# Optimization experiments

Hardware: AMD Instinct MI355X
Metric: run time of the kernel (lower is better)

Reference implementation:

```python
import jax, jax.numpy as jnp
import numpy as np

# ---- static config (mirrors HashEncoderHyFluid.__init__) ----
MIN_RES = np.array([16, 16, 16, 16], dtype=np.float64)
MAX_RES = np.array([256, 256, 256, 128], dtype=np.float64)
NUM_SCALES = 16
MAX_PARAMS = 2 ** 19
F = 2  # features_per_level
N_QUERIES = 1_000_000
PRIMES = np.array([1, 2654435761, 805459861, 3674653429], dtype=np.uint32)
# 16 corner offsets of the 4D hypercube, bit d of idx selects low/high along dim d
BITS = np.array([[(i >> d) & 1 for d in range(4)] for i in range(16)], dtype=np.int32)  # (16,4)


def build_config():
    b = np.exp((np.log(MAX_RES) - np.log(MIN_RES)) / (NUM_SCALES - 1))
    shapes, sizes, indicators, offsets = [], [], [], []
    total = 0
    for s in range(NUM_SCALES):
        res = np.ceil(MIN_RES * np.power(b, s)).astype(np.int64)
        raw = int(res[0] + 1) * int(res[1] + 1) * int(res[2] + 1) * int(res[3] + 1)
        p = raw if raw % 8 == 0 else ((raw + 7) // 8) * 8
        p = min(MAX_PARAMS, p)
        shapes.append(res)
        sizes.append(p)
        indicators.append(1 if raw <= p else 0)
        offsets.append(total)
        total += p * F
    return shapes, sizes, indicators, offsets, total


SHAPES, SIZES, INDICATORS, OFFSETS, TOTAL_HASH_SIZE = build_config()  # total = 15205344


def setup_inputs() -> dict:
    key = jax.random.key(0)
    k1, k2 = jax.random.split(key)
    xyzt = jax.random.uniform(k1, (N_QUERIES, 4), dtype=jnp.float32)  # coords in [0,1)
    hash_table = (jax.random.uniform(k2, (TOTAL_HASH_SIZE,), dtype=jnp.float32) * 2.0 - 1.0) * 0.001
    return {"xyzt": xyzt, "hash_table": hash_table}


def _encode_scale(xyzt, hash_table, res, size, indicator, offset):
    # xyzt: (N,4) in [0,1]; res: np int64 (4,)
    resf = jnp.asarray(res.astype(np.float32))
    pos = xyzt * resf                      # (N,4) grid-space position
    grid = jnp.floor(pos)
    frac = pos - grid                      # (N,4)
    grid = grid.astype(jnp.int32)
    corners = grid[:, None, :] + jnp.asarray(BITS)[None, :, :]          # (N,16,4)
    hi = jnp.asarray(BITS, jnp.float32)[None, :, :]                     # (1,16,4)
    w = jnp.prod(hi * frac[:, None, :] + (1.0 - hi) * (1.0 - frac[:, None, :]), axis=-1)  # (N,16)
    cu = corners.astype(jnp.uint32)
    if indicator == 1:
        # dense linear indexing: strides = cumprod(res+1), wrapping at uint32 like taichi
        strides = np.cumprod(np.concatenate([[1], (res + 1)[:3]])).astype(np.uint32)
        idx = jnp.sum(cu * jnp.asarray(strides), axis=-1)               # (N,16) uint32, wraps
    else:
        # xor hash with large primes
        h = cu[..., 0] * jnp.uint32(PRIMES[0])
        for d in range(1, 4):
            h = h ^ (cu[..., d] * jnp.uint32(PRIMES[d]))
        idx = h
    idx = (idx % jnp.uint32(size)).astype(jnp.int32)
    base = offset + idx * F                                             # (N,16)
    feats = hash_table[base[..., None] + jnp.arange(F)]                 # (N,16,F)
    return jnp.einsum("nc,ncf->nf", w, feats)                           # (N,F)


def reference(xyzt, hash_table):
    outs = []
    for s in range(NUM_SCALES):
        outs.append(_encode_scale(xyzt, hash_table, SHAPES[s], SIZES[s], INDICATORS[s], OFFSETS[s]))
    return jnp.concatenate(outs, axis=-1)  # (N, NUM_SCALES * F)
```

## Files before the change

kernel.cpp:

```cpp
#include <hip/hip_runtime.h>
#include <cstdint>
#include <cmath>


#define NSCALES 16
#define TPB 256
#define BINS 65536
#define QPB 128

struct Cfg {
  float    res[NSCALES][4];
  uint32_t key[NSCALES][4];
  uint32_t mask[NSCALES];
  int      offset[NSCALES];
  int      dense[NSCALES];
};

typedef float v4f __attribute__((ext_vector_type(4)));
typedef float v2f __attribute__((ext_vector_type(2)));

__device__ __forceinline__ uint32_t bucket_key(float x, float y, float z, float w)
{
  uint32_t bx = (uint32_t)(x * 16.f); bx = bx > 15u ? 15u : bx;
  uint32_t by = (uint32_t)(y * 16.f); by = by > 15u ? 15u : by;
  uint32_t bz = (uint32_t)(z * 16.f); bz = bz > 15u ? 15u : bz;
  uint32_t bt = (uint32_t)(w * 16.f); bt = bt > 15u ? 15u : bt;
  uint32_t k = 0;
#pragma unroll
  for (int b = 0; b < 4; ++b) {
    k |= ((bx >> b) & 1u) << (4 * b + 0);
    k |= ((by >> b) & 1u) << (4 * b + 1);
    k |= ((bz >> b) & 1u) << (4 * b + 2);
    k |= ((bt >> b) & 1u) << (4 * b + 3);
  }
  return k;
}

__global__ __launch_bounds__(TPB) void hist_kernel(
    const float* __restrict__ xyzt, uint32_t* __restrict__ hist, int N)
{
  const int i = blockIdx.x * TPB + threadIdx.x;
  if (i >= N) return;
  const v4f c = *(reinterpret_cast<const v4f*>(xyzt) + i);
  atomicAdd(&hist[bucket_key(c.x, c.y, c.z, c.w)], 1u);
}

__global__ __launch_bounds__(1024) void scan_kernel(
    const uint32_t* __restrict__ hist, uint32_t* __restrict__ boff)
{
  __shared__ uint32_t part[1024];
  const int t = threadIdx.x;
  const int base = t * (BINS / 1024);
  uint32_t s = 0;
  for (int j = 0; j < BINS / 1024; ++j) s += hist[base + j];
  part[t] = s;
  __syncthreads();
  for (int off = 1; off < 1024; off <<= 1) {
    uint32_t v = (t >= off) ? part[t - off] : 0u;
    __syncthreads();
    part[t] += v;
    __syncthreads();
  }
  uint32_t run = part[t] - s;
  for (int j = 0; j < BINS / 1024; ++j) {
    boff[base + j] = run;
    run += hist[base + j];
  }
}

__global__ __launch_bounds__(TPB) void scatter_kernel(
    const float* __restrict__ xyzt,
    const uint32_t* __restrict__ boff, uint32_t* __restrict__ cur,
    uint32_t* __restrict__ perm, float* __restrict__ c_sorted, int N)
{
  const int i = blockIdx.x * TPB + threadIdx.x;
  if (i >= N) return;
  const v4f c = *(reinterpret_cast<const v4f*>(xyzt) + i);
  const uint32_t k = bucket_key(c.x, c.y, c.z, c.w);
  const uint32_t pos = boff[k] + atomicAdd(&cur[k], 1u);
  perm[pos] = (uint32_t)i;
  *(reinterpret_cast<v4f*>(c_sorted) + pos) = c;
}

__global__ __launch_bounds__(TPB) void gather_kernel(
    const float*  __restrict__ coords,
    const float*  __restrict__ table,
    float2*       __restrict__ ws,
    int N, int s_base, Cfg cfg)
{
  const int s = (int)blockIdx.y + s_base;
  const int q = blockIdx.x * TPB + threadIdx.x;
  if (q >= N) return;
  const v4f c = *(reinterpret_cast<const v4f*>(coords) + q);

  const float rx = cfg.res[s][0], ry = cfg.res[s][1];
  const float rz = cfg.res[s][2], rw = cfg.res[s][3];
  const uint32_t K0 = cfg.key[s][0], K1 = cfg.key[s][1];
  const uint32_t K2 = cfg.key[s][2], K3 = cfg.key[s][3];

  const float px = c.x * rx, py = c.y * ry, pz = c.z * rz, pw = c.w * rw;
  const float gx = floorf(px), gy = floorf(py), gz = floorf(pz), gw = floorf(pw);
  const float fx = px - gx, fy = py - gy, fz = pz - gz, fw = pw - gw;
  const uint32_t ix = (uint32_t)(int)gx, iy = (uint32_t)(int)gy;
  const uint32_t iz = (uint32_t)(int)gz, iw = (uint32_t)(int)gw;

  const uint32_t x0 = ix * K0, x1 = x0 + K0;
  const uint32_t y0 = iy * K1, y1 = y0 + K1;
  const uint32_t z0 = iz * K2, z1 = z0 + K2;
  const uint32_t u0 = iw * K3, u1 = u0 + K3;

  const float wx0 = 1.f - fx, wy0 = 1.f - fy, wz0 = 1.f - fz, ww0 = 1.f - fw;
  const float wA[4] = { wx0 * wy0, fx * wy0, wx0 * fy, fx * fy };
  const float wB[4] = { wz0 * ww0, fz * ww0, wz0 * fw, fz * fw };

  const float*  tbf = table + cfg.offset[s];
  const float2* __restrict__ tb  = reinterpret_cast<const float2*>(tbf);
  const float4* __restrict__ tb4 = reinterpret_cast<const float4*>(tbf);

  float a0 = 0.f, a1 = 0.f;
  if (cfg.dense[s]) {
    const uint32_t hA[4] = { x0 + y0, x1 + y0, x0 + y1, x1 + y1 };
    const uint32_t hB[4] = { z0 + u0, z1 + u0, z0 + u1, z1 + u1 };
    uint32_t idx[16];
#pragma unroll
    for (int i = 0; i < 16; ++i) idx[i] = hA[i & 3] + hB[i >> 2];
    float2 v[16];
#pragma unroll
    for (int i = 0; i < 16; ++i) v[i] = tb[idx[i]];
#pragma unroll
    for (int i = 0; i < 16; ++i) {
      const float w = wA[i & 3] * wB[i >> 2];
      a0 = fmaf(w, v[i].x, a0);
      a1 = fmaf(w, v[i].y, a1);
    }
  } else {
    const uint32_t msk = cfg.mask[s];
    if ((ix & 1u) == 0u) {
      const uint32_t yv[2] = { y0, y1 };
      const uint32_t zw[4] = { z0 ^ u0, z1 ^ u0, z0 ^ u1, z1 ^ u1 };
      uint32_t p[8];
#pragma unroll
      for (int j = 0; j < 8; ++j)
        p[j] = (x0 ^ yv[j & 1] ^ zw[j >> 1]) & msk;
      float4 v[8];
#pragma unroll
      for (int j = 0; j < 8; ++j) v[j] = tb4[p[j] >> 1];
#pragma unroll
      for (int j = 0; j < 8; ++j) {
        const int jy = j & 1, jz = j >> 1;
        const uint32_t sel = p[j] & 1u;
        const float wlo = wA[2 * jy]     * wB[jz];
        const float whi = wA[2 * jy + 1] * wB[jz];
        const float l0 = sel ? v[j].z : v[j].x, l1 = sel ? v[j].w : v[j].y;
        const float h0 = sel ? v[j].x : v[j].z, h1 = sel ? v[j].y : v[j].w;
        a0 = fmaf(wlo, l0, fmaf(whi, h0, a0));
        a1 = fmaf(wlo, l1, fmaf(whi, h1, a1));
      }
    } else {
      const uint32_t hA[4] = { x0 ^ y0, x1 ^ y0, x0 ^ y1, x1 ^ y1 };
      const uint32_t hB[4] = { z0 ^ u0, z1 ^ u0, z0 ^ u1, z1 ^ u1 };
      uint32_t idx[16];
#pragma unroll
      for (int i = 0; i < 16; ++i) idx[i] = (hA[i & 3] ^ hB[i >> 2]) & msk;
      float2 v[16];
#pragma unroll
      for (int i = 0; i < 16; ++i) v[i] = tb[idx[i]];
#pragma unroll
      for (int i = 0; i < 16; ++i) {
        const float w = wA[i & 3] * wB[i >> 2];
        a0 = fmaf(w, v[i].x, a0);
        a1 = fmaf(w, v[i].y, a1);
      }
    }
  }
  ws[(size_t)s * N + q] = make_float2(a0, a1);
}

__global__ __launch_bounds__(TPB) void transpose_perm(
    const float2*   __restrict__ ws,
    const uint32_t* __restrict__ perm,
    float*          __restrict__ out,
    int N)
{
  __shared__ float2 st[NSCALES][QPB + 1];
  const int t  = threadIdx.x;
  const int q0 = blockIdx.x * QPB;
#pragma unroll
  for (int i = 0; i < (NSCALES * QPB) / TPB; ++i) {
    const int idx = i * TPB + t;
    const int sc  = idx >> 7;
    const int qi  = idx & (QPB - 1);
    const int q   = q0 + qi;
    st[sc][qi] = ws[(size_t)sc * N + (q < N ? q : N - 1)];
  }
  __syncthreads();
#pragma unroll
  for (int i = 0; i < (QPB * 8) / TPB; ++i) {
    const int g  = i * TPB + t;
    const int qi = g >> 3;
    const int h  = g & 7;
    const int q  = q0 + qi;
    if (q < N) {
      const float2 a = st[2 * h][qi];
      const float2 b = st[2 * h + 1][qi];
      const uint32_t pq = perm[q];
      v4f val = { a.x, a.y, b.x, b.y };
      __builtin_nontemporal_store(val, (v4f*)(out + (size_t)pq * 32 + h * 4));
    }
  }
}

__global__ __launch_bounds__(TPB) void transpose_kernel(
    const float2* __restrict__ ws,
    float*        __restrict__ out,
    int N)
{
  __shared__ float2 st[NSCALES][TPB + 1];
  const int t  = threadIdx.x;
  const int q  = blockIdx.x * TPB + t;
  const int ql = q < N ? q : N - 1;
#pragma unroll
  for (int s = 0; s < NSCALES; ++s)
    st[s][t] = ws[(size_t)s * N + ql];
  __syncthreads();
  const int base = blockIdx.x * (TPB * 2 * NSCALES);
#pragma unroll
  for (int it = 0; it < 8; ++it) {
    const int G  = it * 1024 + t * 4;
    const int qi = G >> 5;
    const int s0 = (G & 31) >> 1;
    if (blockIdx.x * TPB + qi < N) {
      const float2 a = st[s0][qi];
      const float2 b = st[s0 + 1][qi];
      v4f val = { a.x, a.y, b.x, b.y };
      __builtin_nontemporal_store(val, (v4f*)(out + base + G));
    }
  }
}

__global__ __launch_bounds__(TPB) void hashenc_fused(
    const float4* __restrict__ xyzt,
    const float*  __restrict__ table,
    float*        __restrict__ out,
    int N, Cfg cfg)
{
  __shared__ float2 st[NSCALES][TPB + 1];
  const int t  = threadIdx.x;
  const int q  = blockIdx.x * TPB + t;
  const int ql = q < N ? q : N - 1;
  const float4 c = xyzt[ql];
#pragma unroll 1
  for (int s = 0; s < NSCALES; ++s) {
    const float rx = cfg.res[s][0], ry = cfg.res[s][1];
    const float rz = cfg.res[s][2], rw = cfg.res[s][3];
    const uint32_t K0 = cfg.key[s][0], K1 = cfg.key[s][1];
    const uint32_t K2 = cfg.key[s][2], K3 = cfg.key[s][3];
    const float px = c.x * rx, py = c.y * ry, pz = c.z * rz, pw = c.w * rw;
    const float gx = floorf(px), gy = floorf(py), gz = floorf(pz), gw = floorf(pw);
    const float fx = px - gx, fy = py - gy, fz = pz - gz, fw = pw - gw;
    const uint32_t ix = (uint32_t)(int)gx, iy = (uint32_t)(int)gy;
    const uint32_t iz = (uint32_t)(int)gz, iw = (uint32_t)(int)gw;
    const uint32_t x0 = ix * K0, x1 = x0 + K0;
    const uint32_t y0 = iy * K1, y1 = y0 + K1;
    const uint32_t z0 = iz * K2, z1 = z0 + K2;
    const uint32_t u0 = iw * K3, u1 = u0 + K3;
    const float wx0 = 1.f - fx, wy0 = 1.f - fy, wz0 = 1.f - fz, ww0 = 1.f - fw;
    const float wA[4] = { wx0 * wy0, fx * wy0, wx0 * fy, fx * fy };
    const float wB[4] = { wz0 * ww0, fz * ww0, wz0 * fw, fz * fw };
    const float2* __restrict__ tb =
        reinterpret_cast<const float2*>(table + cfg.offset[s]);
    float a0 = 0.f, a1 = 0.f;
    if (cfg.dense[s]) {
      const uint32_t hA[4] = { x0 + y0, x1 + y0, x0 + y1, x1 + y1 };
      const uint32_t hB[4] = { z0 + u0, z1 + u0, z0 + u1, z1 + u1 };
#pragma unroll
      for (int i = 0; i < 16; ++i) {
        const uint32_t idx = hA[i & 3] + hB[i >> 2];
        const float2 v = tb[idx];
        const float w = wA[i & 3] * wB[i >> 2];
        a0 = fmaf(w, v.x, a0); a1 = fmaf(w, v.y, a1);
      }
    } else {
      const uint32_t msk = cfg.mask[s];
      const uint32_t hA[4] = { x0 ^ y0, x1 ^ y0, x0 ^ y1, x1 ^ y1 };
      const uint32_t hB[4] = { z0 ^ u0, z1 ^ u0, z0 ^ u1, z1 ^ u1 };
#pragma unroll
      for (int i = 0; i < 16; ++i) {
        const uint32_t idx = (hA[i & 3] ^ hB[i >> 2]) & msk;
        const float2 v = tb[idx];
        const float w = wA[i & 3] * wB[i >> 2];
        a0 = fmaf(w, v.x, a0); a1 = fmaf(w, v.y, a1);
      }
    }
    st[s][t] = make_float2(a0, a1);
  }
  __syncthreads();
  const int base = blockIdx.x * (TPB * 2 * NSCALES);
#pragma unroll
  for (int it = 0; it < 8; ++it) {
    const int G  = it * 1024 + t * 4;
    const int qi = G >> 5;
    const int s0 = (G & 31) >> 1;
    if (blockIdx.x * TPB + qi < N) {
      const float2 a = st[s0][qi];
      const float2 b = st[s0 + 1][qi];
      v4f val = { a.x, a.y, b.x, b.y };
      __builtin_nontemporal_store(val, (v4f*)(out + base + G));
    }
  }
}

static void build_cfg(Cfg& cfg)
{
  const double minr[4] = { 16.0, 16.0, 16.0, 16.0 };
  const double maxr[4] = { 256.0, 256.0, 256.0, 128.0 };
  const uint32_t primes[4] = { 1u, 2654435761u, 805459861u, 3674653429u };

  double b[4];
  for (int d = 0; d < 4; ++d)
    b[d] = ::exp((::log(maxr[d]) - ::log(minr[d])) / (double)(NSCALES - 1));

  long long total = 0;
  for (int s = 0; s < NSCALES; ++s) {
    long long res[4];
    for (int d = 0; d < 4; ++d)
      res[d] = (long long)::ceil(minr[d] * ::pow(b[d], (double)s));

    const long long raw =
        (res[0] + 1) * (res[1] + 1) * (res[2] + 1) * (res[3] + 1);
    long long p = (raw % 8 == 0) ? raw : ((raw + 7) / 8) * 8;
    if (p > 524288) p = 524288;
    const int ind = (raw <= p) ? 1 : 0;

    for (int d = 0; d < 4; ++d) cfg.res[s][d] = (float)res[d];
    if (ind) {
      cfg.key[s][0] = 1u;
      cfg.key[s][1] = (uint32_t)(res[0] + 1);
      cfg.key[s][2] = (uint32_t)((res[0] + 1) * (res[1] + 1));
      cfg.key[s][3] = (uint32_t)((res[0] + 1) * (res[1] + 1) * (res[2] + 1));
    } else {
      for (int d = 0; d < 4; ++d) cfg.key[s][d] = primes[d];
    }
    cfg.mask[s]   = (uint32_t)(p - 1);
    cfg.offset[s] = (int)total;
    cfg.dense[s]  = ind;
    total += p * 2;
  }
}

static inline size_t align_up(size_t v, size_t a) { return (v + a - 1) & ~(a - 1); }

extern "C" void kernel_launch(void* const* d_in, const int* in_sizes, int n_in,
                              void* d_out, int out_size, void* d_ws, size_t ws_size,
                              hipStream_t stream)
{
  const float* xyzt  = (const float*)d_in[0];
  const float* table = (const float*)d_in[1];
  float*       out   = (float*)d_out;
  const int N = in_sizes[0] / 4;

  Cfg cfg;
  build_cfg(cfg);

  const int qblocks = (N + TPB - 1) / TPB;

  size_t off = 0;
  const size_t perm_off = off;             off = align_up(off + (size_t)N * 4, 256);
  const size_t hist_off = off;             off += (size_t)BINS * 4;
  const size_t cur_off  = off;             off = align_up(off + (size_t)BINS * 4, 256);
  const size_t boff_off = off;             off = align_up(off + (size_t)BINS * 4, 256);
  const size_t cs_off   = align_up(off, 16);  off = cs_off + (size_t)N * 16;
  const size_t ws_off   = align_up(off, 16);
  const size_t need_sorted = ws_off + (size_t)N * NSCALES * sizeof(float2);
  const size_t need_plain  = (size_t)N * NSCALES * sizeof(float2);

  char* wsb = (char*)d_ws;

  if (ws_size >= need_sorted) {
    uint32_t* perm = (uint32_t*)(wsb + perm_off);
    uint32_t* hist = (uint32_t*)(wsb + hist_off);
    uint32_t* cur  = (uint32_t*)(wsb + cur_off);
    uint32_t* boff = (uint32_t*)(wsb + boff_off);
    float*    csrt = (float*)(wsb + cs_off);
    float2*   ws   = (float2*)(wsb + ws_off);

    hipMemsetAsync(hist, 0, (size_t)BINS * 8, stream);
    hipLaunchKernelGGL(hist_kernel, dim3(qblocks), dim3(TPB), 0, stream,
                       xyzt, hist, N);
    hipLaunchKernelGGL(scan_kernel, dim3(1), dim3(1024), 0, stream, hist, boff);
    hipLaunchKernelGGL(scatter_kernel, dim3(qblocks), dim3(TPB), 0, stream,
                       xyzt, boff, cur, perm, csrt, N);
    hipLaunchKernelGGL(gather_kernel, dim3(qblocks, NSCALES), dim3(TPB), 0,
                       stream, csrt, table, ws, N, 0, cfg);
    const int tblocks = (N + QPB - 1) / QPB;
    hipLaunchKernelGGL(transpose_perm, dim3(tblocks), dim3(TPB), 0, stream,
                       ws, perm, out, N);
  } else if (ws_size >= need_plain) {
    float2* ws = (float2*)d_ws;
    hipLaunchKernelGGL(gather_kernel, dim3(qblocks, NSCALES), dim3(TPB), 0,
                       stream, xyzt, table, ws, N, 0, cfg);
    hipLaunchKernelGGL(transpose_kernel, dim3(qblocks), dim3(TPB), 0,
                       stream, ws, out, N);
  } else {
    hipLaunchKernelGGL(hashenc_fused, dim3(qblocks), dim3(TPB), 0,
                       stream, (const float4*)xyzt, table, out, N, cfg);
  }
}
```

Baseline: 811.2 us.

## Merge bucket offsets into cursor array, interleave gathers, use nontemporal workspace I/O

The scan now writes exclusive bucket offsets straight into the atomic cursor array, so the scatter no longer reads a separate offset array and the memset shrinks to one histogram. The gather loops now compute each index, load and accumulate in one unrolled body instead of separate phases, which may reduce register pressure. Workspace writes in the gather and reads in the transpose use nontemporal hints to avoid polluting cache that the hash table lookups rely on. The compiler may already hoist the loads, so the loop restructuring could change little.

Result: no change. 808.9 us, median of 2 (-0.3%).

```diff
diff --git a/kernel.cpp b/kernel.cpp
--- a/kernel.cpp
+++ b/kernel.cpp
@@ -46,7 +46,7 @@
 }
 
 __global__ __launch_bounds__(1024) void scan_kernel(
-    const uint32_t* __restrict__ hist, uint32_t* __restrict__ boff)
+    const uint32_t* __restrict__ hist, uint32_t* __restrict__ cur)
 {
   __shared__ uint32_t part[1024];
   const int t = threadIdx.x;
@@ -63,21 +63,21 @@
   }
   uint32_t run = part[t] - s;
   for (int j = 0; j < BINS / 1024; ++j) {
-    boff[base + j] = run;
+    cur[base + j] = run;
     run += hist[base + j];
   }
 }
 
 __global__ __launch_bounds__(TPB) void scatter_kernel(
     const float* __restrict__ xyzt,
-    const uint32_t* __restrict__ boff, uint32_t* __restrict__ cur,
+    uint32_t* __restrict__ cur,
     uint32_t* __restrict__ perm, float* __restrict__ c_sorted, int N)
 {
   const int i = blockIdx.x * TPB + threadIdx.x;
   if (i >= N) return;
   const v4f c = *(reinterpret_cast<const v4f*>(xyzt) + i);
   const uint32_t k = bucket_key(c.x, c.y, c.z, c.w);
-  const uint32_t pos = boff[k] + atomicAdd(&cur[k], 1u);
+  const uint32_t pos = atomicAdd(&cur[k], 1u);
   perm[pos] = (uint32_t)i;
   *(reinterpret_cast<v4f*>(c_sorted) + pos) = c;
 }
@@ -121,59 +121,48 @@
   if (cfg.dense[s]) {
     const uint32_t hA[4] = { x0 + y0, x1 + y0, x0 + y1, x1 + y1 };
     const uint32_t hB[4] = { z0 + u0, z1 + u0, z0 + u1, z1 + u1 };
-    uint32_t idx[16];
-#pragma unroll
-    for (int i = 0; i < 16; ++i) idx[i] = hA[i & 3] + hB[i >> 2];
-    float2 v[16];
-#pragma unroll
-    for (int i = 0; i < 16; ++i) v[i] = tb[idx[i]];
 #pragma unroll
     for (int i = 0; i < 16; ++i) {
+      const uint32_t idx = hA[i & 3] + hB[i >> 2];
+      const float2 v = tb[idx];
       const float w = wA[i & 3] * wB[i >> 2];
-      a0 = fmaf(w, v[i].x, a0);
-      a1 = fmaf(w, v[i].y, a1);
+      a0 = fmaf(w, v.x, a0);
+      a1 = fmaf(w, v.y, a1);
     }
   } else {
     const uint32_t msk = cfg.mask[s];
     if ((ix & 1u) == 0u) {
       const uint32_t yv[2] = { y0, y1 };
       const uint32_t zw[4] = { z0 ^ u0, z1 ^ u0, z0 ^ u1, z1 ^ u1 };
-      uint32_t p[8];
-#pragma unroll
-      for (int j = 0; j < 8; ++j)
-        p[j] = (x0 ^ yv[j & 1] ^ zw[j >> 1]) & msk;
-      float4 v[8];
-#pragma unroll
-      for (int j = 0; j < 8; ++j) v[j] = tb4[p[j] >> 1];
 #pragma unroll
       for (int j = 0; j < 8; ++j) {
         const int jy = j & 1, jz = j >> 1;
-        const uint32_t sel = p[j] & 1u;
+        const uint32_t p  = (x0 ^ yv[jy] ^ zw[jz]) & msk;
+        const uint32_t e  = p & ~1u;
+        const uint32_t sel = p & 1u;
+        const float4 v = tb4[e >> 1];
         const float wlo = wA[2 * jy]     * wB[jz];
         const float whi = wA[2 * jy + 1] * wB[jz];
-        const float l0 = sel ? v[j].z : v[j].x, l1 = sel ? v[j].w : v[j].y;
-        const float h0 = sel ? v[j].x : v[j].z, h1 = sel ? v[j].y : v[j].w;
+        const float l0 = sel ? v.z : v.x, l1 = sel ? v.w : v.y;
+        const float h0 = sel ? v.x : v.z, h1 = sel ? v.y : v.w;
         a0 = fmaf(wlo, l0, fmaf(whi, h0, a0));
         a1 = fmaf(wlo, l1, fmaf(whi, h1, a1));
       }
     } else {
       const uint32_t hA[4] = { x0 ^ y0, x1 ^ y0, x0 ^ y1, x1 ^ y1 };
       const uint32_t hB[4] = { z0 ^ u0, z1 ^ u0, z0 ^ u1, z1 ^ u1 };
-      uint32_t idx[16];
-#pragma unroll
-      for (int i = 0; i < 16; ++i) idx[i] = (hA[i & 3] ^ hB[i >> 2]) & msk;
-      float2 v[16];
-#pragma unroll
-      for (int i = 0; i < 16; ++i) v[i] = tb[idx[i]];
 #pragma unroll
       for (int i = 0; i < 16; ++i) {
+        const uint32_t idx = (hA[i & 3] ^ hB[i >> 2]) & msk;
+        const float2 v = tb[idx];
         const float w = wA[i & 3] * wB[i >> 2];
-        a0 = fmaf(w, v[i].x, a0);
-        a1 = fmaf(w, v[i].y, a1);
+        a0 = fmaf(w, v.x, a0);
+        a1 = fmaf(w, v.y, a1);
       }
     }
   }
-  ws[(size_t)s * N + q] = make_float2(a0, a1);
+  v2f val = { a0, a1 };
+  __builtin_nontemporal_store(val, (v2f*)&ws[(size_t)s * N + q]);
 }
 
 __global__ __launch_bounds__(TPB) void transpose_perm(
@@ -191,7 +180,9 @@
     const int sc  = idx >> 7;
     const int qi  = idx & (QPB - 1);
     const int q   = q0 + qi;
-    st[sc][qi] = ws[(size_t)sc * N + (q < N ? q : N - 1)];
+    const v2f tmp = __builtin_nontemporal_load(
+        reinterpret_cast<const v2f*>(&ws[(size_t)sc * N + (q < N ? q : N - 1)]));
+    st[sc][qi] = make_float2(tmp.x, tmp.y);
   }
   __syncthreads();
 #pragma unroll
@@ -366,9 +357,8 @@
 
   size_t off = 0;
   const size_t perm_off = off;             off = align_up(off + (size_t)N * 4, 256);
-  const size_t hist_off = off;             off += (size_t)BINS * 4;
+  const size_t hist_off = off;             off = align_up(off + (size_t)BINS * 4, 256);
   const size_t cur_off  = off;             off = align_up(off + (size_t)BINS * 4, 256);
-  const size_t boff_off = off;             off = align_up(off + (size_t)BINS * 4, 256);
   const size_t cs_off   = align_up(off, 16);  off = cs_off + (size_t)N * 16;
   const size_t ws_off   = align_up(off, 16);
   const size_t need_sorted = ws_off + (size_t)N * NSCALES * sizeof(float2);
@@ -380,16 +370,15 @@
     uint32_t* perm = (uint32_t*)(wsb + perm_off);
     uint32_t* hist = (uint32_t*)(wsb + hist_off);
     uint32_t* cur  = (uint32_t*)(wsb + cur_off);
-    uint32_t* boff = (uint32_t*)(wsb + boff_off);
     float*    csrt = (float*)(wsb + cs_off);
     float2*   ws   = (float2*)(wsb + ws_off);
 
-    hipMemsetAsync(hist, 0, (size_t)BINS * 8, stream);
+    hipMemsetAsync(hist, 0, (size_t)BINS * 4, stream);
     hipLaunchKernelGGL(hist_kernel, dim3(qblocks), dim3(TPB), 0, stream,
                        xyzt, hist, N);
-    hipLaunchKernelGGL(scan_kernel, dim3(1), dim3(1024), 0, stream, hist, boff);
+    hipLaunchKernelGGL(scan_kernel, dim3(1), dim3(1024), 0, stream, hist, cur);
     hipLaunchKernelGGL(scatter_kernel, dim3(qblocks), dim3(TPB), 0, stream,
-                       xyzt, boff, cur, perm, csrt, N);
+                       xyzt, cur, perm, csrt, N);
     hipLaunchKernelGGL(gather_kernel, dim3(qblocks, NSCALES), dim3(TPB), 0,
                        stream, csrt, table, ws, N, 0, cfg);
     const int tblocks = (N + QPB - 1) / QPB;
```
